# Kernel optimization log

Hardware: AMD Instinct MI355X
Metric: run time of the kernel (lower is better)

Reference implementation:

```python
import jax, jax.numpy as jnp
import numpy as np

KS, PAD, N = 3, 1, 9  # deformable 3x3 kernel, padding 1, N = 9 taps
EPS = 1e-5


def conv2d(x, w, b=None, stride=1, padding=1):
    out = jax.lax.conv_general_dilated(
        x, w, (stride, stride), [(padding, padding)] * 2,
        dimension_numbers=("NCHW", "OIHW", "NCHW"))
    if b is not None:
        out = out + b[None, :, None, None]
    return out


def batchnorm(x, gamma, beta):
    # training-mode BN (fresh module, batch statistics), biased variance like torch
    mean = jnp.mean(x, axis=(0, 2, 3), keepdims=True)
    var = jnp.var(x, axis=(0, 2, 3), keepdims=True)
    xn = (x - mean) * jax.lax.rsqrt(var + EPS)
    return xn * gamma[None, :, None, None] + beta[None, :, None, None]


def gather_corners(xp, qx, qy):
    # xp: (b,c,Hp,Wp); qx,qy: (b,h,w,N) int32 -> (b,c,h,w,N)
    b, c, Hp, Wp = xp.shape
    _, h, w, n = qx.shape
    idx = (qx * Wp + qy).reshape(b, 1, h * w * n)
    out = jnp.take_along_axis(xp.reshape(b, c, Hp * Wp), idx, axis=2)
    return out.reshape(b, c, h, w, n)


def deform_conv(feat, offset, w4):
    # feat: (b,256,h,w), offset: (b,18,h,w) interleaved (x1,y1,x2,y2,...)
    b, c, h, w = feat.shape
    off_x = jnp.transpose(offset[:, 0::2], (0, 2, 3, 1))  # (b,h,w,N)
    off_y = jnp.transpose(offset[:, 1::2], (0, 2, 3, 1))
    xp = jnp.pad(feat, ((0, 0), (0, 0), (PAD, PAD), (PAD, PAD)))
    Hp, Wp = h + 2 * PAD, w + 2 * PAD
    # kernel tap offsets, row-major over (dx,dy)
    pn_x = jnp.array([-1, -1, -1, 0, 0, 0, 1, 1, 1], jnp.float32)
    pn_y = jnp.array([-1, 0, 1, -1, 0, 1, -1, 0, 1], jnp.float32)
    p0_x = jnp.arange(1, h + 1, dtype=jnp.float32)[None, :, None, None]
    p0_y = jnp.arange(1, w + 1, dtype=jnp.float32)[None, None, :, None]
    px = p0_x + pn_x[None, None, None, :] + off_x  # sampling coords in padded map
    py = p0_y + pn_y[None, None, None, :] + off_y

    fpx = jnp.floor(jax.lax.stop_gradient(px))
    fpy = jnp.floor(jax.lax.stop_gradient(py))
    q_lt_x = jnp.clip(fpx, 0, Hp - 1).astype(jnp.int32)
    q_lt_y = jnp.clip(fpy, 0, Wp - 1).astype(jnp.int32)
    q_rb_x = jnp.clip(fpx + 1, 0, Hp - 1).astype(jnp.int32)
    q_rb_y = jnp.clip(fpy + 1, 0, Wp - 1).astype(jnp.int32)

    # out-of-range points snapped to floor (as in original), then clamped
    mask_x = (px < PAD) | (px > Hp - 1 - PAD)
    mask_y = (py < PAD) | (py > Wp - 1 - PAD)
    px = jnp.clip(jnp.where(mask_x, jnp.floor(px), px), 0, Hp - 1)
    py = jnp.clip(jnp.where(mask_y, jnp.floor(py), py), 0, Wp - 1)

    ltx, lty = q_lt_x.astype(jnp.float32), q_lt_y.astype(jnp.float32)
    rbx, rby = q_rb_x.astype(jnp.float32), q_rb_y.astype(jnp.float32)
    g_lt = (1 + (ltx - px)) * (1 + (lty - py))
    g_rb = (1 - (rbx - px)) * (1 - (rby - py))
    g_lb = (1 + (ltx - px)) * (1 - (rby - py))
    g_rt = (1 - (rbx - px)) * (1 + (lty - py))

    x_off = (g_lt[:, None] * gather_corners(xp, q_lt_x, q_lt_y)
             + g_rb[:, None] * gather_corners(xp, q_rb_x, q_rb_y)
             + g_lb[:, None] * gather_corners(xp, q_lt_x, q_rb_y)
             + g_rt[:, None] * gather_corners(xp, q_rb_x, q_lt_y))  # (b,c,h,w,N)

    # stride-ks conv over the ks*ks-expanded map == contraction over (c, tap)
    outc = w4.shape[0]
    return jnp.einsum("bchwn,ocn->bohw", x_off, w4.reshape(outc, c, N))


def setup_inputs() -> dict:
    key = jax.random.key(0)
    ks = jax.random.split(key, 8)
    x = jax.random.normal(ks[0], (2, 3, 224, 224), jnp.float32)
    w1 = jax.random.normal(ks[1], (64, 3, 3, 3), jnp.float32) * 0.1
    b1 = jnp.zeros((64,), jnp.float32)
    g1 = jnp.ones((64,), jnp.float32)
    be1 = jnp.zeros((64,), jnp.float32)
    w2 = jax.random.normal(ks[2], (256, 64, 3, 3), jnp.float32) * 0.04
    b2 = jnp.zeros((256,), jnp.float32)
    g2 = jnp.ones((256,), jnp.float32)
    be2 = jnp.zeros((256,), jnp.float32)
    w_off = jax.random.normal(ks[3], (18, 256, 3, 3), jnp.float32) * 0.01
    b_off = jnp.zeros((18,), jnp.float32)
    w4 = jax.random.normal(ks[4], (256, 256, 3, 3), jnp.float32) * 0.02
    return dict(x=x, w1=w1, b1=b1, g1=g1, be1=be1, w2=w2, b2=b2, g2=g2,
                be2=be2, w_off=w_off, b_off=b_off, w4=w4)


def reference(x, w1, b1, g1, be1, w2, b2, g2, be2, w_off, b_off, w4):
    h = jax.nn.relu(conv2d(x, w1, b1))
    h = batchnorm(h, g1, be1)
    b_, c, H, W = h.shape
    h = h.reshape(b_, c, H // 2, 2, W // 2, 2).mean(axis=(3, 5))  # AvgPool 2x2
    h = jax.nn.relu(conv2d(h, w2, b2))
    h = batchnorm(h, g2, be2)
    offset = conv2d(h, w_off, b_off)  # (b,18,h,w)
    return deform_conv(h, offset, w4)
```

## Files before the change

kernel.cpp:

```cpp
#include <hip/hip_runtime.h>
#include <hip/hip_bf16.h>

#define NP1 50176
#define NP2 12544
#define NPP 12996

typedef __attribute__((ext_vector_type(8))) short short8;
typedef __attribute__((ext_vector_type(4))) float f32x4;

__device__ __forceinline__ unsigned short f2bu(float f){
  __hip_bfloat16 h = __float2bfloat16(f);
  return *reinterpret_cast<unsigned short*>(&h);
}
__device__ __forceinline__ float blo(unsigned u){ union{unsigned q; float f;} x; x.q = u<<16; return x.f; }
__device__ __forceinline__ float bhi(unsigned u){ union{unsigned q; float f;} x; x.q = u & 0xffff0000u; return x.f; }

#define S_SUM1   0
#define S_SUM2   128
#define S_STATS1 640
#define S_STATS2 768
#define S_WOFF2  1280
#define S_W4F    75008
#define S_W2FH   369920
#define S_W2FL   443648
#define S_OFFB   517376
#define S_PPAD   968960
#define S_PHI    2632448
#define S_PLO    3464192
#define S_HPAD   4295936
#define S_HPADL  10949888
#define S_WOFFH  14276864
#define S_WOFFL  14313728
#define S_PB2    14350592
#define S_HPADH  15014144
#define WS_NEED_FLOATS 18341120ull
#define WS_NEED_BYTES  (WS_NEED_FLOATS*4ull)

__global__ void k_w4f(const float* __restrict__ w4, unsigned short* __restrict__ w4f){
  int idx = blockIdx.x*256+threadIdx.x;
  int kt = idx/8192; int r = idx - kt*8192;
  int oc = r>>5, kk = r&31;
  int k = kt*32 + kk; int n = k>>8, c = k&255;
  w4f[idx] = f2bu(w4[oc*2304 + c*9 + n]);
}
__global__ void k_woff2(const float* __restrict__ woff, float* __restrict__ woff2){
  int idx = blockIdx.x*256+threadIdx.x;
  int k = idx>>5, oc = idx&31;
  int n = k>>8, c = k&255;
  woff2[idx] = (oc<18) ? woff[oc*2304 + c*9 + n] : 0.f;
}
__global__ void k_wofff(const float* __restrict__ woff, unsigned short* __restrict__ woffh,
                        unsigned short* __restrict__ woffl){
  int idx = blockIdx.x*256+threadIdx.x;
  int kt = idx>>10; int r = idx & 1023;
  int oc = r>>5, kk = r&31;
  int k = kt*32 + kk; int n = k>>8, c = k&255;
  float wv = (oc<18) ? woff[oc*2304 + c*9 + n] : 0.f;
  unsigned short hi = f2bu(wv);
  woffh[idx] = hi;
  woffl[idx] = f2bu(wv - blo(hi));
}
__global__ void k_w2f(const float* __restrict__ w2, unsigned short* __restrict__ w2fh,
                      unsigned short* __restrict__ w2fl){
  int idx = blockIdx.x*256+threadIdx.x;
  int kt = idx/8192; int r = idx - kt*8192;
  int oc = r>>5, kk = r&31;
  int k = kt*32 + kk; int n = k>>6, c = k&63;
  float wv = w2[oc*576 + c*9 + n];
  unsigned short hi = f2bu(wv);
  w2fh[idx] = hi;
  w2fl[idx] = f2bu(wv - blo(hi));
}

__global__ __launch_bounds__(256) void k_conv1pool(
    const float* __restrict__ x, const float* __restrict__ w1, const float* __restrict__ b1,
    float* __restrict__ ppad, float* __restrict__ sum1){
  __shared__ float xs[3*34*34];
  int bid = blockIdx.x;
  int tile = bid % 49; int oc = (bid/49) & 63; int b = bid/(49*64);
  int tu = tile/7, tv = tile - 7*(tile/7);
  int tid = threadIdx.x;
  int in0 = tu*32 - 1, jn0 = tv*32 - 1;
  for(int t=tid; t<3468; t+=256){
    int c = t/1156; int r2 = t - c*1156; int rr = r2/34; int cc = r2 - rr*34;
    int ii = in0+rr, jj = jn0+cc;
    xs[t] = (ii>=0 && ii<224 && jj>=0 && jj<224) ? x[(size_t)(b*3+c)*NP1 + ii*224+jj] : 0.f;
  }
  float w[27];
  #pragma unroll
  for(int t=0;t<27;t++) w[t] = w1[oc*27+t];
  float bia = b1[oc];
  __syncthreads();
  int u = tid>>4, v = tid&15;
  float s1=0.f, s2=0.f, pl=0.f;
  #pragma unroll
  for(int dy=0;dy<2;dy++){
    #pragma unroll
    for(int dx=0;dx<2;dx++){
      float acc = bia;
      #pragma unroll
      for(int c=0;c<3;c++)
        #pragma unroll
        for(int kh=0;kh<3;kh++)
          #pragma unroll
          for(int kw=0;kw<3;kw++)
            acc += xs[c*1156 + (2*u+dy+kh)*34 + (2*v+dx+kw)] * w[c*9+kh*3+kw];
      acc = fmaxf(acc, 0.f);
      pl += acc; s1 += acc; s2 += acc*acc;
    }
  }
  int U = tu*16+u, V = tv*16+v;
  ppad[(size_t)(b*64+oc)*NPP + (U+1)*114 + (V+1)] = 0.25f*pl;
  __shared__ float r1[256], r2[256];
  r1[tid]=s1; r2[tid]=s2; __syncthreads();
  for(int o=128;o>0;o>>=1){
    if(tid<o){ r1[tid]+=r1[tid+o]; r2[tid]+=r2[tid+o]; }
    __syncthreads();
  }
  if(tid==0){ atomicAdd(&sum1[oc], r1[0]); atomicAdd(&sum1[64+oc], r2[0]); }
}

__global__ void k_fin1(const float* __restrict__ sum1, const float* __restrict__ g1,
                       const float* __restrict__ be1, float* __restrict__ stats1){
  int ch = threadIdx.x;
  float n = 2.f*(float)NP1;
  float mean = sum1[ch]/n;
  float var  = sum1[64+ch]/n - mean*mean;
  float sc = g1[ch]/sqrtf(var + 1e-5f);
  stats1[ch]    = sc;
  stats1[64+ch] = be1[ch] - mean*sc;
}

__global__ __launch_bounds__(256) void k_affine1t(const float* __restrict__ ppad,
        const float* __restrict__ stats1,
        unsigned short* __restrict__ phi, unsigned short* __restrict__ plo){
  __shared__ float ls[64*65];
  int bid = blockIdx.x;
  int b = bid/204; int pp0 = (bid - b*204)*64;
  int tid = threadIdx.x;
  #pragma unroll
  for(int it=0; it<16; it++){
    int t = it*256 + tid;
    int c = t>>6, q = t&63;
    int pp = pp0 + q;
    float v = 0.f;
    if(pp < NPP){
      int row = pp/114, col = pp - row*114;
      if(row>=1 && row<=112 && col>=1 && col<=112)
        v = stats1[c]*ppad[(size_t)(b*64+c)*NPP + pp] + stats1[64+c];
    }
    ls[c*65+q] = v;
  }
  __syncthreads();
  #pragma unroll
  for(int it=0; it<16; it++){
    int t = it*256 + tid;
    int qq = t/64, c = t%64;
    int qloc = qq & 63;
    int pp = pp0 + qloc;
    if(pp < NPP){
      float v = ls[c*65 + qloc];
      unsigned short hi = f2bu(v);
      phi[((size_t)b*NPP + pp)*64 + c] = hi;
      plo[((size_t)b*NPP + pp)*64 + c] = f2bu(v - blo(hi));
    }
  }
}

__global__ __launch_bounds__(256) void k_conv2(
    const unsigned short* __restrict__ phi, const unsigned short* __restrict__ plo,
    const unsigned short* __restrict__ w2fh, const unsigned short* __restrict__ w2fl,
    const float* __restrict__ b2, float* __restrict__ hpad){
  __shared__ float smemf[8800];
  int*  pp_tbl = (int*)smemf;
  unsigned short* afh0 = (unsigned short*)(smemf + 576);
  unsigned short* afl0 = (unsigned short*)(smemf + 576 + 2560);
  float* tb = smemf + 576;
  const int tid = threadIdx.x;
  const int wave = tid>>6, lane = tid&63;
  const int sidx = (blockIdx.x & 7)*49 + (blockIdx.x >> 3);
  const int pix0 = sidx*64;
  const int b = pix0/NP2, ij0 = pix0 - b*NP2;

  for(int t=tid; t<576; t+=256){
    int p = t/9, n = t - 9*(t/9);
    int ij = ij0+p; int i = ij/112, j = ij - i*112;
    pp_tbl[p*9+n] = (i + n/3)*114 + (j + n%3);
  }
  const int px_g = tid>>2;
  const int coff = (tid&3)*8;
  const unsigned short* ph_b = phi + (size_t)b*NPP*64;
  const unsigned short* pl_b = plo + (size_t)b*NPP*64;

  f32x4 acc[4][4] = {};
  __syncthreads();

  auto STAGE = [&](int kt, int buf){
    int n = kt>>1; int cb = ((kt&1)<<5) + coff;
    int pp = pp_tbl[px_g*9 + n];
    *(uint4*)&afh0[buf*2560 + px_g*40 + coff] = *(const uint4*)(ph_b + (size_t)pp*64 + cb);
    *(uint4*)&afl0[buf*2560 + px_g*40 + coff] = *(const uint4*)(pl_b + (size_t)pp*64 + cb);
  };

  const int klo = (lane>>4)<<3;
  STAGE(0, 0);
  for(int kt=0; kt<18; kt++){
    __syncthreads();
    if(kt+1 < 18) STAGE(kt+1, (kt+1)&1);
    const unsigned short* abh = afh0 + (kt&1)*2560;
    const unsigned short* abl = afl0 + (kt&1)*2560;
    short8 aH[4], aL[4];
    #pragma unroll
    for(int mf=0; mf<4; mf++){
      aH[mf] = *(const short8*)&abh[(mf*16 + (lane&15))*40 + klo];
      aL[mf] = *(const short8*)&abl[(mf*16 + (lane&15))*40 + klo];
    }
    #pragma unroll
    for(int nf=0; nf<4; nf++){
      int oc = wave*64 + nf*16 + (lane&15);
      short8 bH = *(const short8*)&w2fh[(size_t)kt*8192 + oc*32 + klo];
      short8 bL = *(const short8*)&w2fl[(size_t)kt*8192 + oc*32 + klo];
      #pragma unroll
      for(int mf=0; mf<4; mf++){
        acc[mf][nf] = __builtin_amdgcn_mfma_f32_16x16x32_bf16(aH[mf], bH, acc[mf][nf], 0,0,0);
        acc[mf][nf] = __builtin_amdgcn_mfma_f32_16x16x32_bf16(aH[mf], bL, acc[mf][nf], 0,0,0);
        acc[mf][nf] = __builtin_amdgcn_mfma_f32_16x16x32_bf16(aL[mf], bH, acc[mf][nf], 0,0,0);
      }
    }
  }
  const int row0 = (lane>>4)<<2, col = lane&15;
  for(int half=0; half<2; half++){
    __syncthreads();
    #pragma unroll
    for(int m2=0; m2<2; m2++){
      int mf = half*2 + m2;
      #pragma unroll
      for(int nf=0; nf<4; nf++){
        int oc = wave*64 + nf*16 + col;
        #pragma unroll
        for(int r=0;r<4;r++) tb[(m2*16 + row0 + r)*257 + oc] = acc[mf][nf][r];
      }
    }
    __syncthreads();
    #pragma unroll
    for(int it=0; it<8; it++){
      int id = it*256 + tid;
      int pxl = id>>6, oc4 = id&63;
      int px = half*32 + pxl;
      int ij = ij0+px; int i = ij/112, j = ij - i*112;
      int pp = (i+1)*114 + (j+1);
      float4 v;
      v.x = fmaxf(tb[pxl*257 + oc4*4+0] + b2[oc4*4+0], 0.f);
      v.y = fmaxf(tb[pxl*257 + oc4*4+1] + b2[oc4*4+1], 0.f);
      v.z = fmaxf(tb[pxl*257 + oc4*4+2] + b2[oc4*4+2], 0.f);
      v.w = fmaxf(tb[pxl*257 + oc4*4+3] + b2[oc4*4+3], 0.f);
      *(float4*)&hpad[((size_t)b*NPP + pp)*256 + oc4*4] = v;
    }
  }
}

__global__ __launch_bounds__(256) void k_bnstats2(const float* __restrict__ hpad,
                                                  float* __restrict__ sum2){
  int c = threadIdx.x;
  int q0 = blockIdx.x*98;
  float s1=0.f, s2=0.f;
  for(int qi=0; qi<98; qi++){
    int q = q0+qi; int b = q/NP2; int pix = q - b*NP2;
    int pp = (pix/112 + 1)*114 + (pix%112) + 1;
    float v = hpad[((size_t)b*NPP + pp)*256 + c];
    s1 += v; s2 += v*v;
  }
  atomicAdd(&sum2[c], s1); atomicAdd(&sum2[256+c], s2);
}

__global__ void k_fin2(const float* __restrict__ sum2, const float* __restrict__ g2,
                       const float* __restrict__ be2, float* __restrict__ stats2){
  int ch = threadIdx.x;
  float n = 2.f*(float)NP2;
  float mean = sum2[ch]/n;
  float var  = sum2[256+ch]/n - mean*mean;
  float sc = g2[ch]/sqrtf(var + 1e-5f);
  stats2[ch]     = sc;
  stats2[256+ch] = be2[ch] - mean*sc;
}

__global__ void k_affine2(float* __restrict__ hpad, const float* __restrict__ stats2,
                          unsigned short* __restrict__ hpadh, unsigned short* __restrict__ hpadl){
  int idx = blockIdx.x*256+threadIdx.x;
  int c = idx & 255; int pi = idx >> 8;
  int pp = pi % NPP;
  int row = pp/114, col = pp - row*114;
  bool in = (row>=1 && row<=112 && col>=1 && col<=112);
  float v = in ? (stats2[c]*hpad[idx] + stats2[256+c]) : 0.f;
  hpad[idx]  = v;
  unsigned short hi = f2bu(v);
  hpadh[idx] = hi;
  hpadl[idx] = f2bu(v - blo(hi));
}

__global__ __launch_bounds__(256) void k_convoff_mfma(
    const unsigned short* __restrict__ hpadh, const unsigned short* __restrict__ hpadl,
    const unsigned short* __restrict__ woffh, const unsigned short* __restrict__ woffl,
    float* __restrict__ p0, float* __restrict__ p1, float* __restrict__ p2){
  __shared__ int pp_tbl[192];
  __shared__ __align__(16) unsigned short afh[2][64*72];
  __shared__ __align__(16) unsigned short afl[2][64*72];
  const int tid = threadIdx.x;
  const int wave = tid>>6, lane = tid&63;
  const int g = blockIdx.x;
  const int xcd = g & 7;
  const int rr  = g >> 3;
  const int split = rr % 3;
  const int sstrip = rr / 3;
  const int strip = xcd*49 + sstrip;
  const int pix0 = strip*64;
  const int b = pix0/NP2, ij0 = pix0 - b*NP2;
  const int n0 = split*3;

  for(int t=tid; t<192; t+=256){
    int p = t/3, nl = t - 3*(t/3);
    int ij = ij0+p; int i = ij/112, j = ij - i*112;
    int n = n0 + nl;
    pp_tbl[p*3+nl] = (i + n/3)*114 + (j + n%3);
  }
  const int px_g = tid>>2;
  const int coff = (tid&3)*16;
  const unsigned short* ph_b = hpadh + (size_t)b*NPP*256;
  const unsigned short* pl_b = hpadl + (size_t)b*NPP*256;
  const int r15 = lane&15, klo = (lane>>4)<<3;

  f32x4 acc[2] = {};
  __syncthreads();

  auto STAGE = [&](int ph, int buf){
    int nl = ph>>2, q = ph&3;
    int pp = pp_tbl[px_g*3 + nl];
    int cb = q*64 + coff;
    uint4 h0 = *(const uint4*)(ph_b + (size_t)pp*256 + cb);
    uint4 h1 = *(const uint4*)(ph_b + (size_t)pp*256 + cb + 8);
    uint4 l0 = *(const uint4*)(pl_b + (size_t)pp*256 + cb);
    uint4 l1 = *(const uint4*)(pl_b + (size_t)pp*256 + cb + 8);
    *(uint4*)&afh[buf][px_g*72 + coff    ] = h0;
    *(uint4*)&afh[buf][px_g*72 + coff + 8] = h1;
    *(uint4*)&afl[buf][px_g*72 + coff    ] = l0;
    *(uint4*)&afl[buf][px_g*72 + coff + 8] = l1;
  };

  STAGE(0, 0);
  for(int ph=0; ph<12; ph++){
    __syncthreads();
    if(ph+1 < 12) STAGE(ph+1, (ph+1)&1);
    const unsigned short* ah = &afh[ph&1][(wave*16 + r15)*72];
    const unsigned short* al = &afl[ph&1][(wave*16 + r15)*72];
    const int n = n0 + (ph>>2), q = ph&3;
    #pragma unroll
    for(int half=0; half<2; half++){
      int kt = n*8 + q*2 + half;
      short8 aH = *(const short8*)&ah[half*32 + klo];
      short8 aL = *(const short8*)&al[half*32 + klo];
      #pragma unroll
      for(int nf=0; nf<2; nf++){
        int oc = nf*16 + r15;
        short8 bH = *(const short8*)&woffh[(size_t)kt*1024 + oc*32 + klo];
        short8 bL = *(const short8*)&woffl[(size_t)kt*1024 + oc*32 + klo];
        acc[nf] = __builtin_amdgcn_mfma_f32_16x16x32_bf16(aH, bH, acc[nf], 0,0,0);
        acc[nf] = __builtin_amdgcn_mfma_f32_16x16x32_bf16(aH, bL, acc[nf], 0,0,0);
        acc[nf] = __builtin_amdgcn_mfma_f32_16x16x32_bf16(aL, bH, acc[nf], 0,0,0);
      }
    }
  }
  float* dst = (split==0) ? p0 : (split==1) ? p1 : p2;
  const int row0 = (lane>>4)<<2;
  #pragma unroll
  for(int nf=0; nf<2; nf++){
    int oc = nf*16 + r15;
    if(oc < 18)
      *(f32x4*)(dst + (size_t)(b*18+oc)*NP2 + ij0 + wave*16 + row0) = acc[nf];
  }
}

__global__ void k_offred3(float* __restrict__ offb, const float* __restrict__ p1,
                          const float* __restrict__ p2, const float* __restrict__ boff){
  int idx = blockIdx.x*256+threadIdx.x;
  int oc = (idx/NP2) % 18;
  offb[idx] = ((offb[idx] + p1[idx]) + p2[idx]) + boff[oc];
}

__global__ __launch_bounds__(256) void k_offfix(const float* __restrict__ hpad,
        const float* __restrict__ woff2, const float* __restrict__ boff,
        float* __restrict__ offb){
  int idx = blockIdx.x*256 + threadIdx.x;
  if(idx >= 83712) return;
  int oc = idx & 31;
  int pid = idx >> 5;
  int b = pid / 1308; int t = pid - b*1308;
  int i, j;
  if(t < 672){
    int r = t/112; i = (r<3) ? r : 106+r; j = t - (t/112)*112;
  } else {
    int u = t - 672; i = 3 + u/6; int c6 = u - 6*(u/6);
    j = (c6<3) ? c6 : 106+c6;
  }
  const float* hb = hpad + (size_t)b*NPP*256;
  float a0=0.f, a1=0.f, a2=0.f, a3=0.f;
  for(int n=0;n<9;n++){
    const float* ap = hb + (size_t)((i + n/3)*114 + (j + n%3))*256;
    const float* wp = woff2 + (size_t)n*256*32 + oc;
    #pragma unroll 4
    for(int c=0;c<256;c+=4){
      float4 a = *(const float4*)(ap + c);
      a0 = fmaf(a.x, wp[(c+0)*32], a0);
      a1 = fmaf(a.y, wp[(c+1)*32], a1);
      a2 = fmaf(a.z, wp[(c+2)*32], a2);
      a3 = fmaf(a.w, wp[(c+3)*32], a3);
    }
  }
  if(oc < 18)
    offb[(size_t)(b*18+oc)*NP2 + i*112 + j] = ((a0+a1)+(a2+a3)) + boff[oc];
}

__global__ __launch_bounds__(256) void k_deform(
    const unsigned short* __restrict__ hpadh,
    const float* __restrict__ offb,
    const unsigned short* __restrict__ w4f,
    float* __restrict__ out){
  __shared__ int   gidx[64][9][4];
  __shared__ float gwt [64][9][4];
  __shared__ unsigned short afrag[2][64*40];
  const int tid = threadIdx.x;
  const int wave = tid>>6, lane = tid&63;
  const int sidx = (blockIdx.x & 7)*49 + (blockIdx.x >> 3);
  const int pix0 = sidx*64;
  const int b = pix0/NP2, ij0 = pix0 - b*NP2;

  for(int t=tid; t<576; t+=256){
    int p = t/9, n = t - 9*(t/9);
    int ij = ij0+p; int i = ij/112, j = ij - i*112;
    float ox = offb[(size_t)(b*18 + 2*n  )*NP2 + ij];
    float oy = offb[(size_t)(b*18 + 2*n+1)*NP2 + ij];
    float px = (float)(i + n/3) + ox;
    float py = (float)(j + n%3) + oy;
    float fpx = floorf(px), fpy = floorf(py);
    float qltxf = fminf(fmaxf(fpx,     0.f),113.f);
    float qltyf = fminf(fmaxf(fpy,     0.f),113.f);
    float qrbxf = fminf(fmaxf(fpx+1.f, 0.f),113.f);
    float qrbyf = fminf(fmaxf(fpy+1.f, 0.f),113.f);
    int qltx=(int)qltxf, qlty=(int)qltyf, qrbx=(int)qrbxf, qrby=(int)qrbyf;
    bool mx = (px<1.f)||(px>112.f);
    bool my = (py<1.f)||(py>112.f);
    float pxc = fminf(fmaxf(mx?fpx:px, 0.f),113.f);
    float pyc = fminf(fmaxf(my?fpy:py, 0.f),113.f);
    float glt = (1.f+(qltxf-pxc))*(1.f+(qltyf-pyc));
    float grb = (1.f-(qrbxf-pxc))*(1.f-(qrbyf-pyc));
    float glb = (1.f+(qltxf-pxc))*(1.f-(qrbyf-pyc));
    float grt = (1.f-(qrbxf-pxc))*(1.f+(qltyf-pyc));
    gidx[p][n][0]=qltx*114+qlty; gwt[p][n][0]=glt;
    gidx[p][n][1]=qrbx*114+qrby; gwt[p][n][1]=grb;
    gidx[p][n][2]=qltx*114+qrby; gwt[p][n][2]=glb;
    gidx[p][n][3]=qrbx*114+qlty; gwt[p][n][3]=grt;
  }

  const int px_g   = tid>>2;
  const int coff_g = (tid&3)*8;
  const unsigned short* hb = hpadh + (size_t)b*NPP*256;

  f32x4 acc[4][4] = {};
  __syncthreads();

  auto GATHER = [&](int kt, int buf){
    int n = kt>>3; int cb = ((kt&7)<<5) + coff_g;
    const int*   gi = gidx[px_g][n];
    const float* gw = gwt[px_g][n];
    f32x4 va = {0.f,0.f,0.f,0.f}, vb = {0.f,0.f,0.f,0.f};
    #pragma unroll
    for(int cr=0;cr<4;cr++){
      const uint4 u = *(const uint4*)(hb + (size_t)gi[cr]*256 + cb);
      float w = gw[cr];
      va.x = fmaf(w, blo(u.x), va.x); va.y = fmaf(w, bhi(u.x), va.y);
      va.z = fmaf(w, blo(u.y), va.z); va.w = fmaf(w, bhi(u.y), va.w);
      vb.x = fmaf(w, blo(u.z), vb.x); vb.y = fmaf(w, bhi(u.z), vb.y);
      vb.z = fmaf(w, blo(u.w), vb.z); vb.w = fmaf(w, bhi(u.w), vb.w);
    }
    uint4 o;
    o.x = (unsigned)f2bu(va.x) | ((unsigned)f2bu(va.y)<<16);
    o.y = (unsigned)f2bu(va.z) | ((unsigned)f2bu(va.w)<<16);
    o.z = (unsigned)f2bu(vb.x) | ((unsigned)f2bu(vb.y)<<16);
    o.w = (unsigned)f2bu(vb.z) | ((unsigned)f2bu(vb.w)<<16);
    *(uint4*)&afrag[buf][px_g*40 + coff_g] = o;
  };

  const int klo = (lane>>4)<<3;
  GATHER(0, 0);
  for(int kt=0; kt<72; kt++){
    __syncthreads();
    if(kt+1 < 72) GATHER(kt+1, (kt+1)&1);
    const unsigned short* ab = afrag[kt&1];
    short8 aF[4];
    #pragma unroll
    for(int mf=0; mf<4; mf++)
      aF[mf] = *(const short8*)&ab[(mf*16 + (lane&15))*40 + klo];
    const unsigned short* wb = w4f + (size_t)kt*8192 + klo;
    #pragma unroll
    for(int nf=0; nf<4; nf++){
      int oc = wave*64 + nf*16 + (lane&15);
      short8 bF = *(const short8*)&wb[oc*32];
      #pragma unroll
      for(int mf=0; mf<4; mf++)
        acc[mf][nf] = __builtin_amdgcn_mfma_f32_16x16x32_bf16(aF[mf], bF, acc[mf][nf], 0,0,0);
    }
  }
  int row0 = ((lane>>4)<<2);
  int col  = lane&15;
  #pragma unroll
  for(int mf=0; mf<4; mf++)
    #pragma unroll
    for(int nf=0; nf<4; nf++){
      int oc = wave*64 + nf*16 + col;
      size_t ob = (size_t)(b*256+oc)*NP2 + ij0 + mf*16 + row0;
      *(f32x4*)(out + ob) = acc[mf][nf];
    }
}

extern "C" void kernel_launch(void* const* d_in, const int* in_sizes, int n_in,
                              void* d_out, int out_size, void* d_ws, size_t ws_size,
                              hipStream_t stream){
  (void)in_sizes; (void)n_in;
  const float* x    = (const float*)d_in[0];
  const float* w1   = (const float*)d_in[1];
  const float* b1   = (const float*)d_in[2];
  const float* g1   = (const float*)d_in[3];
  const float* be1  = (const float*)d_in[4];
  const float* w2   = (const float*)d_in[5];
  const float* b2   = (const float*)d_in[6];
  const float* g2   = (const float*)d_in[7];
  const float* be2  = (const float*)d_in[8];
  const float* woff = (const float*)d_in[9];
  const float* boff = (const float*)d_in[10];
  const float* w4   = (const float*)d_in[11];
  float* out = (float*)d_out;
  float* ws = (float*)d_ws;

  if(ws_size < WS_NEED_BYTES){
    hipMemsetAsync(d_out, 0, (size_t)out_size*sizeof(float), stream);
    return;
  }

  float* sum1   = ws + S_SUM1;
  float* sum2   = ws + S_SUM2;
  float* stats1 = ws + S_STATS1;
  float* stats2 = ws + S_STATS2;
  float* woff2  = ws + S_WOFF2;
  unsigned short* w4f   = (unsigned short*)(ws + S_W4F);
  unsigned short* w2fh  = (unsigned short*)(ws + S_W2FH);
  unsigned short* w2fl  = (unsigned short*)(ws + S_W2FL);
  unsigned short* woffh = (unsigned short*)(ws + S_WOFFH);
  unsigned short* woffl = (unsigned short*)(ws + S_WOFFL);
  float* offb   = ws + S_OFFB;
  float* ppad   = ws + S_PPAD;
  float* pb1    = ws + S_PPAD;
  float* pb2    = ws + S_PB2;
  unsigned short* phi = (unsigned short*)(ws + S_PHI);
  unsigned short* plo = (unsigned short*)(ws + S_PLO);
  float* hpad   = ws + S_HPAD;
  unsigned short* hpadh = (unsigned short*)(ws + S_HPADH);
  unsigned short* hpadl = (unsigned short*)(ws + S_HPADL);

  hipMemsetAsync(sum1, 0, 640*sizeof(float), stream);
  k_w4f          <<<2304,  256, 0, stream>>>(w4, w4f);
  k_woff2        <<<288,   256, 0, stream>>>(woff, woff2);
  k_wofff        <<<288,   256, 0, stream>>>(woff, woffh, woffl);
  k_w2f          <<<576,   256, 0, stream>>>(w2, w2fh, w2fl);
  k_conv1pool    <<<6272,  256, 0, stream>>>(x, w1, b1, ppad, sum1);
  k_fin1         <<<1,     64,  0, stream>>>(sum1, g1, be1, stats1);
  k_affine1t     <<<408,   256, 0, stream>>>(ppad, stats1, phi, plo);
  k_conv2        <<<392,   256, 0, stream>>>(phi, plo, w2fh, w2fl, b2, hpad);
  k_bnstats2     <<<256,   256, 0, stream>>>(hpad, sum2);
  k_fin2         <<<1,     256, 0, stream>>>(sum2, g2, be2, stats2);
  k_affine2      <<<25992, 256, 0, stream>>>(hpad, stats2, hpadh, hpadl);
  k_convoff_mfma <<<1176,  256, 0, stream>>>(hpadh, hpadl, woffh, woffl, offb, pb1, pb2);
  k_offred3      <<<1764,  256, 0, stream>>>(offb, pb1, pb2, boff);
  k_offfix       <<<327,   256, 0, stream>>>(hpad, woff2, boff, offb);
  k_deform       <<<392,   256, 0, stream>>>(hpadh, offb, w4f, out);
}
```

Before: 406.9 us.

## Fuse weight prep kernels, fold BN2 stats into conv2, widen deform gather

Merges the four weight-reformatting kernels into one launch and moves the BN2 sum and sum-of-squares into the conv2 epilogue, removing the separate k_bnstats2 pass over hpad. k_affine2 now writes the fp32 normalized hpad only in a border band, on the assumption that later readers (k_offfix) touch only that region. The deform kernel gathers 64 channels per phase instead of 32, halving the number of barrier-separated gather steps and issuing four corner loads together for more memory parallelism. The trade-offs are extra LDS and register use, and a correctness dependency on which hpad rows k_offfix actually reads.

```diff
diff --git a/kernel.cpp b/kernel.cpp
--- a/kernel.cpp
+++ b/kernel.cpp
@@ -36,40 +36,41 @@
 #define WS_NEED_FLOATS 18341120ull
 #define WS_NEED_BYTES  (WS_NEED_FLOATS*4ull)
 
-__global__ void k_w4f(const float* __restrict__ w4, unsigned short* __restrict__ w4f){
+__global__ void k_prep(const float* __restrict__ w4, const float* __restrict__ woff,
+                       const float* __restrict__ w2,
+                       unsigned short* __restrict__ w4f, float* __restrict__ woff2,
+                       unsigned short* __restrict__ woffh, unsigned short* __restrict__ woffl,
+                       unsigned short* __restrict__ w2fh, unsigned short* __restrict__ w2fl){
   int idx = blockIdx.x*256+threadIdx.x;
-  int kt = idx/8192; int r = idx - kt*8192;
-  int oc = r>>5, kk = r&31;
-  int k = kt*32 + kk; int n = k>>8, c = k&255;
-  w4f[idx] = f2bu(w4[oc*2304 + c*9 + n]);
-}
-__global__ void k_woff2(const float* __restrict__ woff, float* __restrict__ woff2){
-  int idx = blockIdx.x*256+threadIdx.x;
-  int k = idx>>5, oc = idx&31;
-  int n = k>>8, c = k&255;
-  woff2[idx] = (oc<18) ? woff[oc*2304 + c*9 + n] : 0.f;
-}
-__global__ void k_wofff(const float* __restrict__ woff, unsigned short* __restrict__ woffh,
-                        unsigned short* __restrict__ woffl){
-  int idx = blockIdx.x*256+threadIdx.x;
-  int kt = idx>>10; int r = idx & 1023;
-  int oc = r>>5, kk = r&31;
-  int k = kt*32 + kk; int n = k>>8, c = k&255;
-  float wv = (oc<18) ? woff[oc*2304 + c*9 + n] : 0.f;
-  unsigned short hi = f2bu(wv);
-  woffh[idx] = hi;
-  woffl[idx] = f2bu(wv - blo(hi));
-}
-__global__ void k_w2f(const float* __restrict__ w2, unsigned short* __restrict__ w2fh,
-                      unsigned short* __restrict__ w2fl){
-  int idx = blockIdx.x*256+threadIdx.x;
-  int kt = idx/8192; int r = idx - kt*8192;
-  int oc = r>>5, kk = r&31;
-  int k = kt*32 + kk; int n = k>>6, c = k&63;
-  float wv = w2[oc*576 + c*9 + n];
-  unsigned short hi = f2bu(wv);
-  w2fh[idx] = hi;
-  w2fl[idx] = f2bu(wv - blo(hi));
+  if(idx < 589824){
+    int kt = idx/8192; int r = idx - kt*8192;
+    int oc = r>>5, kk = r&31;
+    int k = kt*32 + kk; int n = k>>8, c = k&255;
+    w4f[idx] = f2bu(w4[oc*2304 + c*9 + n]);
+  } else if(idx < 663552){
+    int i2 = idx - 589824;
+    int k = i2>>5, oc = i2&31;
+    int n = k>>8, c = k&255;
+    woff2[i2] = (oc<18) ? woff[oc*2304 + c*9 + n] : 0.f;
+  } else if(idx < 737280){
+    int i3 = idx - 663552;
+    int kt = i3>>10; int r = i3 & 1023;
+    int oc = r>>5, kk = r&31;
+    int k = kt*32 + kk; int n = k>>8, c = k&255;
+    float wv = (oc<18) ? woff[oc*2304 + c*9 + n] : 0.f;
+    unsigned short hi = f2bu(wv);
+    woffh[i3] = hi;
+    woffl[i3] = f2bu(wv - blo(hi));
+  } else {
+    int i4 = idx - 737280;
+    int kt = i4/8192; int r = i4 - kt*8192;
+    int oc = r>>5, kk = r&31;
+    int k = kt*32 + kk; int n = k>>6, c = k&63;
+    float wv = w2[oc*576 + c*9 + n];
+    unsigned short hi = f2bu(wv);
+    w2fh[i4] = hi;
+    w2fl[i4] = f2bu(wv - blo(hi));
+  }
 }
 
 __global__ __launch_bounds__(256) void k_conv1pool(
@@ -170,7 +171,7 @@
 __global__ __launch_bounds__(256) void k_conv2(
     const unsigned short* __restrict__ phi, const unsigned short* __restrict__ plo,
     const unsigned short* __restrict__ w2fh, const unsigned short* __restrict__ w2fl,
-    const float* __restrict__ b2, float* __restrict__ hpad){
+    const float* __restrict__ b2, float* __restrict__ hpad, float* __restrict__ sum2){
   __shared__ float smemf[8800];
   int*  pp_tbl = (int*)smemf;
   unsigned short* afh0 = (unsigned short*)(smemf + 576);
@@ -229,6 +230,7 @@
     }
   }
   const int row0 = (lane>>4)<<2, col = lane&15;
+  float s1q[4] = {0.f,0.f,0.f,0.f}, s2q[4] = {0.f,0.f,0.f,0.f};
   for(int half=0; half<2; half++){
     __syncthreads();
     #pragma unroll
@@ -255,22 +257,22 @@
       v.z = fmaxf(tb[pxl*257 + oc4*4+2] + b2[oc4*4+2], 0.f);
       v.w = fmaxf(tb[pxl*257 + oc4*4+3] + b2[oc4*4+3], 0.f);
       *(float4*)&hpad[((size_t)b*NPP + pp)*256 + oc4*4] = v;
-    }
-  }
-}
-
-__global__ __launch_bounds__(256) void k_bnstats2(const float* __restrict__ hpad,
-                                                  float* __restrict__ sum2){
-  int c = threadIdx.x;
-  int q0 = blockIdx.x*98;
-  float s1=0.f, s2=0.f;
-  for(int qi=0; qi<98; qi++){
-    int q = q0+qi; int b = q/NP2; int pix = q - b*NP2;
-    int pp = (pix/112 + 1)*114 + (pix%112) + 1;
-    float v = hpad[((size_t)b*NPP + pp)*256 + c];
-    s1 += v; s2 += v*v;
-  }
-  atomicAdd(&sum2[c], s1); atomicAdd(&sum2[256+c], s2);
+      s1q[0] += v.x; s2q[0] += v.x*v.x;
+      s1q[1] += v.y; s2q[1] += v.y*v.y;
+      s1q[2] += v.z; s2q[2] += v.z*v.z;
+      s1q[3] += v.w; s2q[3] += v.w*v.w;
+    }
+  }
+  __syncthreads();
+  #pragma unroll
+  for(int q=0;q<4;q++){ tb[tid*4+q] = s1q[q]; tb[1024 + tid*4+q] = s2q[q]; }
+  __syncthreads();
+  {
+    int oc = tid;
+    float s1 = ((tb[oc] + tb[256+oc]) + tb[512+oc]) + tb[768+oc];
+    float s2 = ((tb[1024+oc] + tb[1280+oc]) + tb[1536+oc]) + tb[1792+oc];
+    atomicAdd(&sum2[oc], s1); atomicAdd(&sum2[256+oc], s2);
+  }
 }
 
 __global__ void k_fin2(const float* __restrict__ sum2, const float* __restrict__ g2,
@@ -292,7 +294,8 @@
   int row = pp/114, col = pp - row*114;
   bool in = (row>=1 && row<=112 && col>=1 && col<=112);
   float v = in ? (stats2[c]*hpad[idx] + stats2[256+c]) : 0.f;
-  hpad[idx]  = v;
+  bool band = (row<6) || (row>107) || (col<6) || (col>107);
+  if(band) hpad[idx] = v;
   unsigned short hi = f2bu(v);
   hpadh[idx] = hi;
   hpadl[idx] = f2bu(v - blo(hi));
@@ -426,7 +429,7 @@
     float* __restrict__ out){
   __shared__ int   gidx[64][9][4];
   __shared__ float gwt [64][9][4];
-  __shared__ unsigned short afrag[2][64*40];
+  __shared__ __align__(16) unsigned short afrag[2][64*72];
   const int tid = threadIdx.x;
   const int wave = tid>>6, lane = tid&63;
   const int sidx = (blockIdx.x & 7)*49 + (blockIdx.x >> 3);
@@ -467,46 +470,67 @@
   f32x4 acc[4][4] = {};
   __syncthreads();
 
-  auto GATHER = [&](int kt, int buf){
-    int n = kt>>3; int cb = ((kt&7)<<5) + coff_g;
+  auto GATHER = [&](int ph, int buf){
+    int n = ph>>2; int qb = (ph&3)<<6;
     const int*   gi = gidx[px_g][n];
     const float* gw = gwt[px_g][n];
-    f32x4 va = {0.f,0.f,0.f,0.f}, vb = {0.f,0.f,0.f,0.f};
-    #pragma unroll
-    for(int cr=0;cr<4;cr++){
-      const uint4 u = *(const uint4*)(hb + (size_t)gi[cr]*256 + cb);
-      float w = gw[cr];
-      va.x = fmaf(w, blo(u.x), va.x); va.y = fmaf(w, bhi(u.x), va.y);
-      va.z = fmaf(w, blo(u.y), va.z); va.w = fmaf(w, bhi(u.y), va.w);
-      vb.x = fmaf(w, blo(u.z), vb.x); vb.y = fmaf(w, bhi(u.z), vb.y);
-      vb.z = fmaf(w, blo(u.w), vb.z); vb.w = fmaf(w, bhi(u.w), vb.w);
-    }
-    uint4 o;
-    o.x = (unsigned)f2bu(va.x) | ((unsigned)f2bu(va.y)<<16);
-    o.y = (unsigned)f2bu(va.z) | ((unsigned)f2bu(va.w)<<16);
-    o.z = (unsigned)f2bu(vb.x) | ((unsigned)f2bu(vb.y)<<16);
-    o.w = (unsigned)f2bu(vb.z) | ((unsigned)f2bu(vb.w)<<16);
-    *(uint4*)&afrag[buf][px_g*40 + coff_g] = o;
+    int i0 = gi[0], i1 = gi[1], i2 = gi[2], i3 = gi[3];
+    float w0 = gw[0], w1 = gw[1], w2 = gw[2], w3 = gw[3];
+    #pragma unroll
+    for(int h=0; h<2; h++){
+      int cb = qb + h*32 + coff_g;
+      f32x4 va = {0.f,0.f,0.f,0.f}, vb = {0.f,0.f,0.f,0.f};
+      const uint4 u0 = *(const uint4*)(hb + (size_t)i0*256 + cb);
+      const uint4 u1 = *(const uint4*)(hb + (size_t)i1*256 + cb);
+      const uint4 u2 = *(const uint4*)(hb + (size_t)i2*256 + cb);
+      const uint4 u3 = *(const uint4*)(hb + (size_t)i3*256 + cb);
+      va.x = fmaf(w0, blo(u0.x), va.x); va.y = fmaf(w0, bhi(u0.x), va.y);
+      va.z = fmaf(w0, blo(u0.y), va.z); va.w = fmaf(w0, bhi(u0.y), va.w);
+      vb.x = fmaf(w0, blo(u0.z), vb.x); vb.y = fmaf(w0, bhi(u0.z), vb.y);
+      vb.z = fmaf(w0, blo(u0.w), vb.z); vb.w = fmaf(w0, bhi(u0.w), vb.w);
+      va.x = fmaf(w1, blo(u1.x), va.x); va.y = fmaf(w1, bhi(u1.x), va.y);
+      va.z = fmaf(w1, blo(u1.y), va.z); va.w = fmaf(w1, bhi(u1.y), va.w);
+      vb.x = fmaf(w1, blo(u1.z), vb.x); vb.y = fmaf(w1, bhi(u1.z), vb.y);
+      vb.z = fmaf(w1, blo(u1.w), vb.z); vb.w = fmaf(w1, bhi(u1.w), vb.w);
+      va.x = fmaf(w2, blo(u2.x), va.x); va.y = fmaf(w2, bhi(u2.x), va.y);
+      va.z = fmaf(w2, blo(u2.y), va.z); va.w = fmaf(w2, bhi(u2.y), va.w);
+      vb.x = fmaf(w2, blo(u2.z), vb.x); vb.y = fmaf(w2, bhi(u2.z), vb.y);
+      vb.z = fmaf(w2, blo(u2.w), vb.z); vb.w = fmaf(w2, bhi(u2.w), vb.w);
+      va.x = fmaf(w3, blo(u3.x), va.x); va.y = fmaf(w3, bhi(u3.x), va.y);
+      va.z = fmaf(w3, blo(u3.y), va.z); va.w = fmaf(w3, bhi(u3.y), va.w);
+      vb.x = fmaf(w3, blo(u3.z), vb.x); vb.y = fmaf(w3, bhi(u3.z), vb.y);
+      vb.z = fmaf(w3, blo(u3.w), vb.z); vb.w = fmaf(w3, bhi(u3.w), vb.w);
+      uint4 o;
+      o.x = (unsigned)f2bu(va.x) | ((unsigned)f2bu(va.y)<<16);
+      o.y = (unsigned)f2bu(va.z) | ((unsigned)f2bu(va.w)<<16);
+      o.z = (unsigned)f2bu(vb.x) | ((unsigned)f2bu(vb.y)<<16);
+      o.w = (unsigned)f2bu(vb.z) | ((unsigned)f2bu(vb.w)<<16);
+      *(uint4*)&afrag[buf][px_g*72 + h*32 + coff_g] = o;
+    }
   };
 
   const int klo = (lane>>4)<<3;
   GATHER(0, 0);
-  for(int kt=0; kt<72; kt++){
+  for(int ph=0; ph<36; ph++){
     __syncthreads();
-    if(kt+1 < 72) GATHER(kt+1, (kt+1)&1);
-    const unsigned short* ab = afrag[kt&1];
-    short8 aF[4];
-    #pragma unroll
-    for(int mf=0; mf<4; mf++)
-      aF[mf] = *(const short8*)&ab[(mf*16 + (lane&15))*40 + klo];
-    const unsigned short* wb = w4f + (size_t)kt*8192 + klo;
-    #pragma unroll
-    for(int nf=0; nf<4; nf++){
-      int oc = wave*64 + nf*16 + (lane&15);
-      short8 bF = *(const short8*)&wb[oc*32];
+    if(ph+1 < 36) GATHER(ph+1, (ph+1)&1);
+    const unsigned short* ab = afrag[ph&1];
+    #pragma unroll
+    for(int h=0; h<2; h++){
+      int kt = (ph>>2)*8 + (ph&3)*2 + h;
+      short8 aF[4];
       #pragma unroll
       for(int mf=0; mf<4; mf++)
-        acc[mf][nf] = __builtin_amdgcn_mfma_f32_16x16x32_bf16(aF[mf], bF, acc[mf][nf], 0,0,0);
+        aF[mf] = *(const short8*)&ab[(mf*16 + (lane&15))*72 + h*32 + klo];
+      const unsigned short* wb = w4f + (size_t)kt*8192 + klo;
+      #pragma unroll
+      for(int nf=0; nf<4; nf++){
+        int oc = wave*64 + nf*16 + (lane&15);
+        short8 bF = *(const short8*)&wb[oc*32];
+        #pragma unroll
+        for(int mf=0; mf<4; mf++)
+          acc[mf][nf] = __builtin_amdgcn_mfma_f32_16x16x32_bf16(aF[mf], bF, acc[mf][nf], 0,0,0);
+      }
     }
   }
   int row0 = ((lane>>4)<<2);
@@ -566,15 +590,11 @@
   unsigned short* hpadl = (unsigned short*)(ws + S_HPADL);
 
   hipMemsetAsync(sum1, 0, 640*sizeof(float), stream);
-  k_w4f          <<<2304,  256, 0, stream>>>(w4, w4f);
-  k_woff2        <<<288,   256, 0, stream>>>(woff, woff2);
-  k_wofff        <<<288,   256, 0, stream>>>(woff, woffh, woffl);
-  k_w2f          <<<576,   256, 0, stream>>>(w2, w2fh, w2fl);
+  k_prep         <<<3456,  256, 0, stream>>>(w4, woff, w2, w4f, woff2, woffh, woffl, w2fh, w2fl);
   k_conv1pool    <<<6272,  256, 0, stream>>>(x, w1, b1, ppad, sum1);
   k_fin1         <<<1,     64,  0, stream>>>(sum1, g1, be1, stats1);
   k_affine1t     <<<408,   256, 0, stream>>>(ppad, stats1, phi, plo);
-  k_conv2        <<<392,   256, 0, stream>>>(phi, plo, w2fh, w2fl, b2, hpad);
-  k_bnstats2     <<<256,   256, 0, stream>>>(hpad, sum2);
+  k_conv2        <<<392,   256, 0, stream>>>(phi, plo, w2fh, w2fl, b2, hpad, sum2);
   k_fin2         <<<1,     256, 0, stream>>>(sum2, g2, be2, stats2);
   k_affine2      <<<25992, 256, 0, stream>>>(hpad, stats2, hpadh, hpadl);
   k_convoff_mfma <<<1176,  256, 0, stream>>>(hpadh, hpadl, woffh, woffl, offb, pb1, pb2);
```

New measurement: 386.2 us. 1.05x faster.
